# Performance work log

Hardware: AMD Instinct MI355X
Metric: run time of the kernel (lower is better)

The kernel has to match this reference:

```python
import jax, jax.numpy as jnp
import numpy as np


def setup_inputs() -> dict:
    key = jax.random.key(0)
    ks = jax.random.split(key, 4)
    B, T, D, H = 64, 512, 512, 1024
    return {
        "x": jax.random.normal(ks[0], (B, T, D), dtype=jnp.float32),
        "kz": jax.random.normal(ks[1], (D, H), dtype=jnp.float32) * (1.0 / np.sqrt(D)),
        "kr": jax.random.normal(ks[2], (D, H), dtype=jnp.float32) * (1.0 / np.sqrt(D)),
        "kh": jax.random.normal(ks[3], (D, H), dtype=jnp.float32) * (1.0 / np.sqrt(D)),
        "mz": jnp.ones((H,), dtype=jnp.float32),
        "mr": jnp.ones((H,), dtype=jnp.float32),
        "br": jnp.zeros((H,), dtype=jnp.float32),
        "bz": jnp.zeros((H,), dtype=jnp.float32),
    }


def reference(x, kz, kr, kh, mz, mr, br, bz):
    B, T, D = x.shape
    H = kz.shape[1]
    # Precompute input projections for all timesteps (batched GEMMs),
    # identical math to per-step matmuls in the original cell.
    xz = jnp.einsum("btd,dh->bth", x, kz)  # [B,T,H]
    xr = jnp.einsum("btd,dh->bth", x, kr)
    xh = jnp.einsum("btd,dh->bth", x, kh)

    def step(h, inp):
        xz_t, xr_t, xh_t = inp  # each [B,H]
        r = jnp.tanh(xr_t + h * mr + br) + 1.0
        z = jax.nn.sigmoid(xz_t + h * mz + bz)
        h_new = z * h + (1.0 - z) * jnp.tanh(xh_t + r * h)
        return h_new, h_new

    h0 = jnp.zeros((B, H), dtype=x.dtype)
    # scan over time axis: move T to leading dim
    xs = (jnp.swapaxes(xz, 0, 1), jnp.swapaxes(xr, 0, 1), jnp.swapaxes(xh, 0, 1))
    _, ys = jax.lax.scan(step, h0, xs)  # ys: [T,B,H]
    return jnp.swapaxes(ys, 0, 1)  # [B,T,H]
```

## Files before the change

### kernel.cpp

```cpp
#include <hip/hip_runtime.h>
#include <hip/hip_bf16.h>
#include <math.h>


#define M_DIM 32768
#define K_DIM 512
#define H_DIM 1024
#define N3    3072

typedef _Float16 half8v __attribute__((ext_vector_type(8)));
typedef _Float16 half4v __attribute__((ext_vector_type(4)));
typedef float f32x4 __attribute__((ext_vector_type(4)));

__device__ __forceinline__ f32x4 mfma16(half8v a, half8v b, f32x4 c) {
    return __builtin_amdgcn_mfma_f32_16x16x32_f16(a, b, c, 0, 0, 0);
}

__device__ __forceinline__ void load_lds16(const void* g, void* l) {
    __builtin_amdgcn_global_load_lds(
        (const __attribute__((address_space(1))) void*)g,
        (__attribute__((address_space(3))) void*)l, 16, 0, 0);
}

__global__ __launch_bounds__(256) void convert_x(
    const float4* __restrict__ x4, half4v* __restrict__ hi4,
    half4v* __restrict__ lo4, int n4)
{
    int i = blockIdx.x * 256 + threadIdx.x;
    if (i >= n4) return;
    float4 v = x4[i];
    half4v h, lo;
    h.x = (_Float16)v.x; lo.x = (_Float16)(v.x - (float)h.x);
    h.y = (_Float16)v.y; lo.y = (_Float16)(v.y - (float)h.y);
    h.z = (_Float16)v.z; lo.z = (_Float16)(v.z - (float)h.z);
    h.w = (_Float16)v.w; lo.w = (_Float16)(v.w - (float)h.w);
    hi4[i] = h; lo4[i] = lo;
}

__global__ __launch_bounds__(256) void convert_wt(
    const float* __restrict__ kz, const float* __restrict__ kr,
    const float* __restrict__ kh, _Float16* __restrict__ wth,
    _Float16* __restrict__ wtl)
{
    int gid = blockIdx.x * 256 + threadIdx.x;
    int k = gid & (K_DIM - 1);
    int n = (gid >> 9) & (H_DIM - 1);
    int wsel = gid >> 19;
    const float* s = (wsel == 0) ? kz : ((wsel == 1) ? kr : kh);
    float v = s[(size_t)k * H_DIM + n];
    _Float16 h = (_Float16)v;
    wth[gid] = h;
    wtl[gid] = (_Float16)(v - (float)h);
}

__global__ __launch_bounds__(512, 2) void gemm_mfma_split(
    const _Float16* __restrict__ Ahi, const _Float16* __restrict__ Alo,
    const _Float16* __restrict__ Bthi, const _Float16* __restrict__ Btlo,
    float* __restrict__ XZ, float* __restrict__ XR, float* __restrict__ OUT)
{
    __shared__ _Float16 AT[2][256 * 64];
    __shared__ _Float16 BT[2][256 * 64];

    const int tid = threadIdx.x;
    const int w = tid >> 6, l = tid & 63;
    const int l15 = l & 15, quad = l >> 4;
    const int wr = w >> 2;
    const int wc = w & 3;

    const int nblk = blockIdx.x;
    const int swz = (nblk & 7) * 192 + (nblk >> 3);
    const int by = swz / 12;
    const int bx = swz - by * 12;
    const long m0 = (long)by * 256;
    const long n0 = (long)bx * 256;

    f32x4 acc[8][4] = {};

    const _Float16* gA[4]; const _Float16* gB[4];
    int lofs[4];
#pragma unroll
    for (int i = 0; i < 4; ++i) {
        const int s = i * 512 + tid;
        const int r = s >> 3;
        const int o2 = ((s & 7) ^ (r & 7)) << 4;
        const int part  = o2 >> 6;
        const int khalf = ((o2 >> 4) & 3) * 8;
        gA[i] = (part ? Alo : Ahi) + (m0 + r) * K_DIM + khalf;
        gB[i] = (part ? Btlo : Bthi) + (n0 + r) * K_DIM + khalf;
        lofs[i] = (i * 512 + (w << 6)) * 8;
    }

#pragma unroll
    for (int i = 0; i < 4; ++i) { load_lds16(gA[i], &AT[0][lofs[i]]); gA[i] += 32; }
#pragma unroll
    for (int i = 0; i < 4; ++i) { load_lds16(gB[i], &BT[0][lofs[i]]); gB[i] += 32; }
    asm volatile("s_waitcnt vmcnt(0)" ::: "memory");
    __builtin_amdgcn_s_barrier();

    int cur = 0;
    for (int t = 0; t < 16; ++t) {
        const bool pf = (t + 1) < 16;
        const _Float16* at = &AT[cur][0];
        const _Float16* bt = &BT[cur][0];
        _Float16* an = &AT[cur ^ 1][0];
        _Float16* bn = &BT[cur ^ 1][0];

        half8v bfh[4], bfl[4], afh[4], afl[4];
#pragma unroll
        for (int ni = 0; ni < 4; ++ni) {
            const int r = wc * 64 + ni * 16 + l15;
            const int off = (quad ^ (r & 7)) * 8;
            bfh[ni] = *(const half8v*)&bt[r * 64 + off];
            bfl[ni] = *(const half8v*)&bt[r * 64 + (off ^ 32)];
        }
#pragma unroll
        for (int mi = 0; mi < 4; ++mi) {
            const int r = wr * 128 + mi * 16 + l15;
            const int off = (quad ^ (r & 7)) * 8;
            afh[mi] = *(const half8v*)&at[r * 64 + off];
            afl[mi] = *(const half8v*)&at[r * 64 + (off ^ 32)];
        }
        if (pf) {
#pragma unroll
            for (int i = 0; i < 4; ++i) { load_lds16(gA[i], an + lofs[i]); gA[i] += 32; }
        }
        __builtin_amdgcn_s_barrier();
        asm volatile("s_waitcnt lgkmcnt(0)" ::: "memory");
        __builtin_amdgcn_sched_barrier(0);
        __builtin_amdgcn_s_setprio(1);
#pragma unroll
        for (int mi = 0; mi < 4; ++mi)
#pragma unroll
            for (int ni = 0; ni < 4; ++ni)
                acc[mi][ni] = mfma16(afh[mi], bfh[ni], acc[mi][ni]);
#pragma unroll
        for (int mi = 0; mi < 4; ++mi)
#pragma unroll
            for (int ni = 0; ni < 4; ++ni)
                acc[mi][ni] = mfma16(afh[mi], bfl[ni], acc[mi][ni]);
#pragma unroll
        for (int mi = 0; mi < 4; ++mi)
#pragma unroll
            for (int ni = 0; ni < 4; ++ni)
                acc[mi][ni] = mfma16(afl[mi], bfh[ni], acc[mi][ni]);
        __builtin_amdgcn_s_setprio(0);
        __builtin_amdgcn_s_barrier();

        half8v afh2[4], afl2[4];
#pragma unroll
        for (int mi = 0; mi < 4; ++mi) {
            const int r = wr * 128 + 64 + mi * 16 + l15;
            const int off = (quad ^ (r & 7)) * 8;
            afh2[mi] = *(const half8v*)&at[r * 64 + off];
            afl2[mi] = *(const half8v*)&at[r * 64 + (off ^ 32)];
        }
        if (pf) {
#pragma unroll
            for (int i = 0; i < 4; ++i) { load_lds16(gB[i], bn + lofs[i]); gB[i] += 32; }
        }
        __builtin_amdgcn_s_barrier();
        asm volatile("s_waitcnt lgkmcnt(0)" ::: "memory");
        __builtin_amdgcn_sched_barrier(0);
        __builtin_amdgcn_s_setprio(1);
#pragma unroll
        for (int mi = 0; mi < 4; ++mi)
#pragma unroll
            for (int ni = 0; ni < 4; ++ni)
                acc[4 + mi][ni] = mfma16(afh2[mi], bfh[ni], acc[4 + mi][ni]);
#pragma unroll
        for (int mi = 0; mi < 4; ++mi)
#pragma unroll
            for (int ni = 0; ni < 4; ++ni)
                acc[4 + mi][ni] = mfma16(afh2[mi], bfl[ni], acc[4 + mi][ni]);
#pragma unroll
        for (int mi = 0; mi < 4; ++mi)
#pragma unroll
            for (int ni = 0; ni < 4; ++ni)
                acc[4 + mi][ni] = mfma16(afl2[mi], bfh[ni], acc[4 + mi][ni]);
        __builtin_amdgcn_s_setprio(0);
        asm volatile("s_waitcnt vmcnt(0)" ::: "memory");
        __builtin_amdgcn_s_barrier();
        cur ^= 1;
    }

    float* dst = (bx < 4) ? XZ : ((bx < 8) ? XR : OUT);
    const long nl = (long)(bx & 3) * 256 + wc * 64 + l15;
#pragma unroll
    for (int mi = 0; mi < 8; ++mi) {
        const long m = m0 + wr * 128 + mi * 16 + quad * 4;
#pragma unroll
        for (int ni = 0; ni < 4; ++ni) {
            float* p = dst + m * H_DIM + nl + ni * 16;
#pragma unroll
            for (int i = 0; i < 4; ++i)
                p[(long)i * H_DIM] = acc[mi][ni][i];
        }
    }
}

#define BM 128
#define BN 128
#define BK 8
__global__ __launch_bounds__(256) void gemm_f32(
    const float* __restrict__ A, const float* __restrict__ B,
    float* __restrict__ C, int M, int N, int K)
{
    __shared__ float As[BK][BM];
    __shared__ float Bs[BK][BN];
    const int tid = threadIdx.x;
    const int bm = blockIdx.y * BM, bn = blockIdx.x * BN;
    const int tx = tid & 15, ty = tid >> 4;
    float acc[8][8];
#pragma unroll
    for (int i = 0; i < 8; i++)
#pragma unroll
        for (int j = 0; j < 8; j++) acc[i][j] = 0.f;
    const int a_row = tid >> 1, a_k = (tid & 1) * 4;
    const int b_row = tid >> 5, b_col = (tid & 31) * 4;
    const float* Aptr = A + (size_t)(bm + a_row) * K + a_k;
    const float* Bptr = B + (size_t)b_row * N + bn + b_col;
    for (int k0 = 0; k0 < K; k0 += BK) {
        float4 av = *(const float4*)(Aptr + k0);
        float4 bv = *(const float4*)(Bptr + (size_t)k0 * N);
        As[a_k + 0][a_row] = av.x; As[a_k + 1][a_row] = av.y;
        As[a_k + 2][a_row] = av.z; As[a_k + 3][a_row] = av.w;
        *(float4*)&Bs[b_row][b_col] = bv;
        __syncthreads();
#pragma unroll
        for (int kk = 0; kk < BK; kk++) {
            float4 a0 = *(const float4*)&As[kk][ty * 8];
            float4 a1 = *(const float4*)&As[kk][ty * 8 + 4];
            float4 b0 = *(const float4*)&Bs[kk][tx * 8];
            float4 b1 = *(const float4*)&Bs[kk][tx * 8 + 4];
            float a[8] = {a0.x, a0.y, a0.z, a0.w, a1.x, a1.y, a1.z, a1.w};
            float b[8] = {b0.x, b0.y, b0.z, b0.w, b1.x, b1.y, b1.z, b1.w};
#pragma unroll
            for (int i = 0; i < 8; i++)
#pragma unroll
                for (int j = 0; j < 8; j++)
                    acc[i][j] = fmaf(a[i], b[j], acc[i][j]);
        }
        __syncthreads();
    }
    float* Cptr = C + (size_t)(bm + ty * 8) * N + bn + tx * 8;
#pragma unroll
    for (int i = 0; i < 8; i++) {
        float4 c0 = {acc[i][0], acc[i][1], acc[i][2], acc[i][3]};
        float4 c1 = {acc[i][4], acc[i][5], acc[i][6], acc[i][7]};
        *(float4*)(Cptr + (size_t)i * N)     = c0;
        *(float4*)(Cptr + (size_t)i * N + 4) = c1;
    }
}

__device__ __forceinline__ float fast_tanh(float x) {
    return 1.0f - 2.0f / (__expf(2.0f * x) + 1.0f);
}
__device__ __forceinline__ float fast_sigmoid(float x) {
    return 1.0f / (1.0f + __expf(-x));
}

__global__ __launch_bounds__(256) void scan_kernel(
    const float* __restrict__ XZ, const float* __restrict__ XR,
    float* __restrict__ OUT,
    const float* __restrict__ mz, const float* __restrict__ mr,
    const float* __restrict__ br, const float* __restrict__ bz)
{
    const int gid = blockIdx.x * blockDim.x + threadIdx.x;
    const int b = gid >> 10;
    const int h = gid & (H_DIM - 1);

    const float mzv = mz[h], mrv = mr[h], brv = br[h], bzv = bz[h];
    float hs = 0.f;
    size_t idx = (size_t)b * 512 * H_DIM + h;

    float cz[16], cr[16], ch[16];
#pragma unroll
    for (int j = 0; j < 16; ++j) {
        cz[j] = XZ[idx + (size_t)j * H_DIM];
        cr[j] = XR[idx + (size_t)j * H_DIM];
        ch[j] = OUT[idx + (size_t)j * H_DIM];
    }
    for (int t0 = 0; t0 < 512; t0 += 16) {
        float nz[16], nr[16], nh[16];
        const bool more = (t0 + 16) < 512;
        const size_t nidx = idx + 16ul * H_DIM;
        if (more) {
#pragma unroll
            for (int j = 0; j < 16; ++j) {
                nz[j] = XZ[nidx + (size_t)j * H_DIM];
                nr[j] = XR[nidx + (size_t)j * H_DIM];
                nh[j] = OUT[nidx + (size_t)j * H_DIM];
            }
        }
#pragma unroll
        for (int j = 0; j < 16; ++j) {
            const float r = fast_tanh(fmaf(hs, mrv, cr[j]) + brv) + 1.0f;
            const float z = fast_sigmoid(fmaf(hs, mzv, cz[j]) + bzv);
            const float hn = fmaf(z, hs, (1.0f - z) * fast_tanh(fmaf(r, hs, ch[j])));
            OUT[idx + (size_t)j * H_DIM] = hn;
            hs = hn;
        }
        idx = nidx;
        if (more) {
#pragma unroll
            for (int j = 0; j < 16; ++j) { cz[j] = nz[j]; cr[j] = nr[j]; ch[j] = nh[j]; }
        }
    }
}

extern "C" void kernel_launch(void* const* d_in, const int* in_sizes, int n_in,
                              void* d_out, int out_size, void* d_ws, size_t ws_size,
                              hipStream_t stream) {
    const float* x  = (const float*)d_in[0];
    const float* kz = (const float*)d_in[1];
    const float* kr = (const float*)d_in[2];
    const float* kh = (const float*)d_in[3];
    const float* mz = (const float*)d_in[4];
    const float* mr = (const float*)d_in[5];
    const float* br = (const float*)d_in[6];
    const float* bz = (const float*)d_in[7];
    float* out = (float*)d_out;

    char* ws = (char*)d_ws;
    float* XZ = (float*)ws;
    float* XR = (float*)(ws + 134217728ul);
    _Float16* XHI = (_Float16*)(ws + 268435456ul);
    _Float16* XLO = (_Float16*)(ws + 301989888ul);
    _Float16* WTH = (_Float16*)(ws + 335544320ul);
    _Float16* WTL = (_Float16*)(ws + 338690048ul);
    const size_t need = 341835776ul;

    if (ws_size >= need) {
        int n4 = M_DIM * K_DIM / 4;
        convert_x<<<n4 / 256, 256, 0, stream>>>(
            (const float4*)x, (half4v*)XHI, (half4v*)XLO, n4);
        convert_wt<<<(3 * H_DIM * K_DIM) / 256, 256, 0, stream>>>(
            kz, kr, kh, WTH, WTL);
        gemm_mfma_split<<<1536, 512, 0, stream>>>(
            XHI, XLO, WTH, WTL, XZ, XR, out);
    } else {
        dim3 grid(H_DIM / BN, M_DIM / BM);
        gemm_f32<<<grid, 256, 0, stream>>>(x, kz, XZ,  M_DIM, H_DIM, K_DIM);
        gemm_f32<<<grid, 256, 0, stream>>>(x, kr, XR,  M_DIM, H_DIM, K_DIM);
        gemm_f32<<<grid, 256, 0, stream>>>(x, kh, out, M_DIM, H_DIM, K_DIM);
    }

    scan_kernel<<<(64 * H_DIM) / 256, 256, 0, stream>>>(
        XZ, XR, out, mz, mr, br, bz);
}
```

Measured before the change: 609.3 us.

## Restructure GEMM LDS prefetch barriers and refactor scan gate math with fast reciprocals

The GEMM main loop now issues both A and B global-to-LDS prefetches at the start of each K-step and drops the two intra-step barriers and waitcnts, keeping only the end-of-step wait and barrier. This is meant to cut synchronisation stalls. In the scan kernel, the gate constants and inputs are pre-scaled and negated so each tanh and sigmoid becomes an exp plus a Newton-refined hardware reciprocal instead of an IEEE division, shortening the serial per-step dependency chain. Dropping the barrier after the LDS fragment reads is safe only because the prefetch writes the other buffer; the scan's numerics change slightly.

```diff
diff --git a/kernel.cpp b/kernel.cpp
--- a/kernel.cpp
+++ b/kernel.cpp
@@ -97,15 +97,21 @@
     asm volatile("s_waitcnt vmcnt(0)" ::: "memory");
     __builtin_amdgcn_s_barrier();
 
-    int cur = 0;
     for (int t = 0; t < 16; ++t) {
-        const bool pf = (t + 1) < 16;
+        const int cur = t & 1;
         const _Float16* at = &AT[cur][0];
         const _Float16* bt = &BT[cur][0];
-        _Float16* an = &AT[cur ^ 1][0];
-        _Float16* bn = &BT[cur ^ 1][0];
-
-        half8v bfh[4], bfl[4], afh[4], afl[4];
+
+        if (t + 1 < 16) {
+            _Float16* an = &AT[cur ^ 1][0];
+            _Float16* bn = &BT[cur ^ 1][0];
+#pragma unroll
+            for (int i = 0; i < 4; ++i) { load_lds16(gA[i], an + lofs[i]); gA[i] += 32; }
+#pragma unroll
+            for (int i = 0; i < 4; ++i) { load_lds16(gB[i], bn + lofs[i]); gB[i] += 32; }
+        }
+
+        half8v bfh[4], bfl[4];
 #pragma unroll
         for (int ni = 0; ni < 4; ++ni) {
             const int r = wc * 64 + ni * 16 + l15;
@@ -113,6 +119,7 @@
             bfh[ni] = *(const half8v*)&bt[r * 64 + off];
             bfl[ni] = *(const half8v*)&bt[r * 64 + (off ^ 32)];
         }
+        half8v afh[4], afl[4];
 #pragma unroll
         for (int mi = 0; mi < 4; ++mi) {
             const int r = wr * 128 + mi * 16 + l15;
@@ -120,13 +127,6 @@
             afh[mi] = *(const half8v*)&at[r * 64 + off];
             afl[mi] = *(const half8v*)&at[r * 64 + (off ^ 32)];
         }
-        if (pf) {
-#pragma unroll
-            for (int i = 0; i < 4; ++i) { load_lds16(gA[i], an + lofs[i]); gA[i] += 32; }
-        }
-        __builtin_amdgcn_s_barrier();
-        asm volatile("s_waitcnt lgkmcnt(0)" ::: "memory");
-        __builtin_amdgcn_sched_barrier(0);
         __builtin_amdgcn_s_setprio(1);
 #pragma unroll
         for (int mi = 0; mi < 4; ++mi)
@@ -144,7 +144,6 @@
             for (int ni = 0; ni < 4; ++ni)
                 acc[mi][ni] = mfma16(afl[mi], bfh[ni], acc[mi][ni]);
         __builtin_amdgcn_s_setprio(0);
-        __builtin_amdgcn_s_barrier();
 
         half8v afh2[4], afl2[4];
 #pragma unroll
@@ -154,13 +153,6 @@
             afh2[mi] = *(const half8v*)&at[r * 64 + off];
             afl2[mi] = *(const half8v*)&at[r * 64 + (off ^ 32)];
         }
-        if (pf) {
-#pragma unroll
-            for (int i = 0; i < 4; ++i) { load_lds16(gB[i], bn + lofs[i]); gB[i] += 32; }
-        }
-        __builtin_amdgcn_s_barrier();
-        asm volatile("s_waitcnt lgkmcnt(0)" ::: "memory");
-        __builtin_amdgcn_sched_barrier(0);
         __builtin_amdgcn_s_setprio(1);
 #pragma unroll
         for (int mi = 0; mi < 4; ++mi)
@@ -178,9 +170,9 @@
             for (int ni = 0; ni < 4; ++ni)
                 acc[4 + mi][ni] = mfma16(afl2[mi], bfh[ni], acc[4 + mi][ni]);
         __builtin_amdgcn_s_setprio(0);
+
         asm volatile("s_waitcnt vmcnt(0)" ::: "memory");
         __builtin_amdgcn_s_barrier();
-        cur ^= 1;
     }
 
     float* dst = (bx < 4) ? XZ : ((bx < 8) ? XR : OUT);
@@ -252,11 +244,9 @@
     }
 }
 
-__device__ __forceinline__ float fast_tanh(float x) {
-    return 1.0f - 2.0f / (__expf(2.0f * x) + 1.0f);
-}
-__device__ __forceinline__ float fast_sigmoid(float x) {
-    return 1.0f / (1.0f + __expf(-x));
+__device__ __forceinline__ float vrcp_nr(float d) {
+    float r = __builtin_amdgcn_rcpf(d);
+    return r * fmaf(-d, r, 2.0f);
 }
 
 __global__ __launch_bounds__(256) void scan_kernel(
@@ -269,16 +259,19 @@
     const int b = gid >> 10;
     const int h = gid & (H_DIM - 1);
 
-    const float mzv = mz[h], mrv = mr[h], brv = br[h], bzv = bz[h];
+    const float mzK = -mz[h];
+    const float mrK = -2.0f * mr[h];
+    const float bzK = -bz[h];
+    const float brK = -2.0f * br[h];
     float hs = 0.f;
     size_t idx = (size_t)b * 512 * H_DIM + h;
 
     float cz[16], cr[16], ch[16];
 #pragma unroll
     for (int j = 0; j < 16; ++j) {
-        cz[j] = XZ[idx + (size_t)j * H_DIM];
-        cr[j] = XR[idx + (size_t)j * H_DIM];
-        ch[j] = OUT[idx + (size_t)j * H_DIM];
+        cz[j] = bzK - XZ[idx + (size_t)j * H_DIM];
+        cr[j] = fmaf(-2.0f, XR[idx + (size_t)j * H_DIM], brK);
+        ch[j] = -2.0f * OUT[idx + (size_t)j * H_DIM];
     }
     for (int t0 = 0; t0 < 512; t0 += 16) {
         float nz[16], nr[16], nh[16];
@@ -294,16 +287,29 @@
         }
 #pragma unroll
         for (int j = 0; j < 16; ++j) {
-            const float r = fast_tanh(fmaf(hs, mrv, cr[j]) + brv) + 1.0f;
-            const float z = fast_sigmoid(fmaf(hs, mzv, cz[j]) + bzv);
-            const float hn = fmaf(z, hs, (1.0f - z) * fast_tanh(fmaf(r, hs, ch[j])));
+            const float u1   = fmaf(hs, mrK, cr[j]);
+            const float uz   = fmaf(hs, mzK, cz[j]);
+            const float hsK2 = -4.0f * hs;
+            const float e1 = __expf(u1);
+            const float s1 = vrcp_nr(e1 + 1.0f);
+            const float ez = __expf(uz);
+            const float sz = vrcp_nr(ez + 1.0f);
+            const float u2 = fmaf(s1, hsK2, ch[j]);
+            const float e2 = __expf(u2);
+            const float s2 = vrcp_nr(e2 + 1.0f);
+            const float th = fmaf(2.0f, s2, -1.0f);
+            const float hn = fmaf(sz, hs - th, th);
             OUT[idx + (size_t)j * H_DIM] = hn;
             hs = hn;
         }
         idx = nidx;
         if (more) {
 #pragma unroll
-            for (int j = 0; j < 16; ++j) { cz[j] = nz[j]; cr[j] = nr[j]; ch[j] = nh[j]; }
+            for (int j = 0; j < 16; ++j) {
+                cz[j] = bzK - nz[j];
+                cr[j] = fmaf(-2.0f, nr[j], brK);
+                ch[j] = -2.0f * nh[j];
+            }
         }
     }
 }
```

After: 586.8 us. 3.7% less time.
